# Kernel optimization log

Hardware: AMD Instinct MI355X
Metric: run time of the kernel (lower is better)

The kernel has to match this reference:

```python
import jax, jax.numpy as jnp
import numpy as np

BN_EPS = 1e-5
L2_EPS = 1e-12  # F.normalize eps


def _phi(x, w, gamma, beta, mean, var):
    # 1x1x1 conv (pointwise channel mix) + BatchNorm3d (inference) + ReLU
    # x: (B, C, T, H, W), w: (L, C) -> (B, L, T, H, W)
    y = jnp.einsum('bcthw,lc->blthw', x, w)
    scale = gamma * jax.lax.rsqrt(var + BN_EPS)
    shift = beta - mean * scale
    y = y * scale[None, :, None, None, None] + shift[None, :, None, None, None]
    return jax.nn.relu(y)


def _l2norm(x, axis):
    n = jnp.sqrt(jnp.sum(x * x, axis=axis, keepdims=True))
    return x / jnp.maximum(n, L2_EPS)


def setup_inputs() -> dict:
    key = jax.random.key(0)
    ks = jax.random.split(key, 8)
    B, C, T, H, W = 8, 512, 8, 28, 28
    L = 64
    inp = {
        'query_feature': jax.random.normal(ks[0], (B, C, T, H, W), jnp.float32),
        'key_feature': jax.random.normal(ks[1], (B, C, T, H, W), jnp.float32),
        'phi_w': jax.random.normal(ks[2], (L, C), jnp.float32) * (1.0 / np.sqrt(C)),
        'phi_gamma': jnp.ones((L,), jnp.float32),
        'phi_beta': jnp.zeros((L,), jnp.float32),
        'phi_mean': jax.random.normal(ks[3], (L,), jnp.float32) * 0.1,
        'phi_var': jax.random.uniform(ks[4], (L,), jnp.float32, 0.5, 1.5),
        'phip_w': jax.random.normal(ks[5], (L, C), jnp.float32) * (1.0 / np.sqrt(C)),
        'phip_gamma': jnp.ones((L,), jnp.float32),
        'phip_beta': jnp.zeros((L,), jnp.float32),
        'phip_mean': jax.random.normal(ks[6], (L,), jnp.float32) * 0.1,
        'phip_var': jax.random.uniform(ks[7], (L,), jnp.float32, 0.5, 1.5),
    }
    return inp


def reference(query_feature, key_feature, phi_w, phi_gamma, phi_beta, phi_mean, phi_var,
              phip_w, phip_gamma, phip_beta, phip_mean, phip_var):
    B, C, T, Hk, Wk = key_feature.shape
    _, _, _, Hq, Wq = query_feature.shape
    Nk = T * Hk * Wk
    Nq = T * Hq * Wq

    # visible -> latent adjacency, L2-normalized over spatial-temporal nodes
    a_v2l = _phi(key_feature, phi_w, phi_gamma, phi_beta, phi_mean, phi_var)
    a_v2l = _l2norm(a_v2l.reshape(B, -1, Nk), axis=2)              # (B, L, Nk)

    k = key_feature.reshape(B, C, Nk)
    latent = jnp.einsum('bln,bcn->blc', a_v2l, k)                   # (B, L, C)

    ln = _l2norm(latent, axis=-1)
    aff = jax.nn.softmax(jnp.einsum('blc,bmc->blm', ln, ln), axis=-1)  # (B, L, L)
    latent = jnp.einsum('blm,bmc->blc', aff, latent)                # (B, L, C)

    # latent -> visible adjacency, L2-normalized over latent dim
    a_l2v = _phi(query_feature, phip_w, phip_gamma, phip_beta, phip_mean, phip_var)
    a_l2v = _l2norm(a_l2v.reshape(B, -1, Nq), axis=1)               # (B, L, Nq)

    out = jnp.einsum('blc,bln->bcn', latent, a_l2v)                 # (B, C, Nq)
    return out.reshape(B, C, T, Hq, Wq)
```

## Files before the change

### kernel.cpp

```cpp
#include <hip/hip_runtime.h>
#include <stdint.h>
#include <stddef.h>

#define NB 8
#define NC 512
#define NL 64
#define NN 6272
#define NT 64
#define NTILES (NN / NT)
#define NTA 32
#define NTILES32 (NN / NTA)
#define NCHUNK 14
#define NSUB (NTILES32 / NCHUNK)

typedef short bf16x8 __attribute__((ext_vector_type(8)));
typedef float f32x4 __attribute__((ext_vector_type(4)));

__device__ __forceinline__ unsigned short f2bf(float f) {
    uint32_t u = __float_as_uint(f);
    u += 0x7fffu + ((u >> 16) & 1u);
    return (unsigned short)(u >> 16);
}
__device__ __forceinline__ float bf2f(unsigned short s) {
    return __uint_as_float(((uint32_t)s) << 16);
}

__global__ __launch_bounds__(512)
void kW(const float* __restrict__ w0, const float* __restrict__ w1,
        unsigned short* __restrict__ f0, unsigned short* __restrict__ f1) {
    const float* src = blockIdx.x ? w1 : w0;
    unsigned short* dst = blockIdx.x ? f1 : f0;
    int t = threadIdx.x;
    #pragma unroll
    for (int j = 0; j < 8; j++) {
        int chunk = t + j * 512;
        int r = chunk & 15, q = (chunk >> 4) & 3, it = (chunk >> 6) & 15, lg = chunk >> 10;
        const float* sp = src + (size_t)(lg * 16 + r) * NC + it * 32 + q * 8;
        float4 x = *(const float4*)sp;
        float4 y = *(const float4*)(sp + 4);
        bf16x8 o;
        o[0] = (short)f2bf(x.x); o[1] = (short)f2bf(x.y);
        o[2] = (short)f2bf(x.z); o[3] = (short)f2bf(x.w);
        o[4] = (short)f2bf(y.x); o[5] = (short)f2bf(y.y);
        o[6] = (short)f2bf(y.z); o[7] = (short)f2bf(y.w);
        *(bf16x8*)(dst + (size_t)chunk * 8) = o;
    }
}

__global__ __launch_bounds__(512, 2)
void kAP(const float* __restrict__ key, const unsigned short* __restrict__ wfA,
         const float* __restrict__ gmaA, const float* __restrict__ btaA,
         const float* __restrict__ muA, const float* __restrict__ varA,
         float* __restrict__ part, float* __restrict__ ssqp,
         const float* __restrict__ query, const unsigned short* __restrict__ wfP,
         const float* __restrict__ gmaP, const float* __restrict__ btaP,
         const float* __restrict__ muP, const float* __restrict__ varP,
         unsigned short* __restrict__ a2T) {
    extern __shared__ char smem[];
    const int id = blockIdx.x;
    const int nA = NCHUNK * NB;
    const int tid = threadIdx.x;
    const int w = tid >> 6;
    const int lane = tid & 63;
    const int q = lane >> 4;
    const int r = lane & 15;
    const f32x4 fz = {0.f, 0.f, 0.f, 0.f};

    if (id < nA) {
        unsigned short* Knc = (unsigned short*)smem;
        unsigned short* Kcn = (unsigned short*)(smem + 33280);
        unsigned short* A1  = (unsigned short*)(smem + 74240);
        float* sc = (float*)(smem + 79360);
        float* sh = sc + NL;

        const int chunk = id % NCHUNK;
        const int b     = id / NCHUNK;
        const int n0    = chunk * (NSUB * NTA);

        if (tid < NL) {
            float s = gmaA[tid] * rsqrtf(varA[tid] + 1e-5f);
            sc[tid] = s;
            sh[tid] = btaA[tid] - muA[tid] * s;
        }

        const int l0  = (w & 3) * 16;
        const int nc0 = (w >> 2) * 16;
        const int c0  = w * 64;
        const int na = nc0 + r;
        const int ga = (na >> 2) & 7;
        const unsigned short* wfp = wfA + ((size_t)((w & 3) * 1024 + q * 16 + r)) * 8;

        const int i4  = tid & 7;
        const int cb0 = tid >> 3;
        const float* kpb = key + (size_t)b * NC * NN + n0;

        uint2 pr[8];
        #pragma unroll
        for (int p = 0; p < 8; p++) {
            float4 v = *(const float4*)(kpb + (size_t)(cb0 + 64 * p) * NN + i4 * 4);
            pr[p].x = (uint32_t)f2bf(v.x) | ((uint32_t)f2bf(v.y) << 16);
            pr[p].y = (uint32_t)f2bf(v.z) | ((uint32_t)f2bf(v.w) << 16);
        }

        f32x4 acc2[4][4];
        #pragma unroll
        for (int fm = 0; fm < 4; fm++)
            #pragma unroll
            for (int fc = 0; fc < 4; fc++) acc2[fm][fc] = fz;
        float s_acc = 0.f;

        for (int s = 0; s < NSUB; s++) {
            __syncthreads();

            #pragma unroll
            for (int p = 0; p < 8; p++) {
                int c = cb0 + 64 * p;
                *(uint2*)&Kcn[c * 40 + i4 * 4] = pr[p];
                int cs = (((c >> 3) ^ i4) << 3) | (c & 7);
                int j = i4 * 4;
                Knc[(j + 0) * 520 + cs] = (unsigned short)(pr[p].x);
                Knc[(j + 1) * 520 + cs] = (unsigned short)(pr[p].x >> 16);
                Knc[(j + 2) * 520 + cs] = (unsigned short)(pr[p].y);
                Knc[(j + 3) * 520 + cs] = (unsigned short)(pr[p].y >> 16);
            }
            __syncthreads();

            if (s + 1 < NSUB) {
                const float* kp = kpb + (s + 1) * NTA;
                #pragma unroll
                for (int p = 0; p < 8; p++) {
                    float4 v = *(const float4*)(kp + (size_t)(cb0 + 64 * p) * NN + i4 * 4);
                    pr[p].x = (uint32_t)f2bf(v.x) | ((uint32_t)f2bf(v.y) << 16);
                    pr[p].y = (uint32_t)f2bf(v.z) | ((uint32_t)f2bf(v.w) << 16);
                }
            }

            {
                f32x4 acc0 = fz;
                #pragma unroll
                for (int it = 0; it < 16; it++) {
                    bf16x8 af = *(const bf16x8*)&wfp[it * 512];
                    bf16x8 b0 = *(const bf16x8*)&Knc[na * 520 + (((it * 4 + q) ^ ga) << 3)];
                    acc0 = __builtin_amdgcn_mfma_f32_16x16x32_bf16(b0, af, acc0, 0, 0, 0);
                }
                const int l = l0 + r;
                const float scl = sc[l], shf = sh[l];
                ushort4 t;
                float v0 = fmaxf(acc0[0] * scl + shf, 0.f);
                float v1 = fmaxf(acc0[1] * scl + shf, 0.f);
                float v2 = fmaxf(acc0[2] * scl + shf, 0.f);
                float v3 = fmaxf(acc0[3] * scl + shf, 0.f);
                t.x = f2bf(v0); t.y = f2bf(v1); t.z = f2bf(v2); t.w = f2bf(v3);
                s_acc += v0 * v0 + v1 * v1 + v2 * v2 + v3 * v3;
                *(ushort4*)&A1[l * 40 + nc0 + q * 4] = t;
            }
            __syncthreads();

            {
                bf16x8 a[4];
                #pragma unroll
                for (int fm = 0; fm < 4; fm++)
                    a[fm] = *(const bf16x8*)&A1[(fm * 16 + r) * 40 + q * 8];
                #pragma unroll
                for (int fc = 0; fc < 4; fc++) {
                    bf16x8 bb = *(const bf16x8*)&Kcn[(c0 + fc * 16 + r) * 40 + q * 8];
                    #pragma unroll
                    for (int fm = 0; fm < 4; fm++)
                        acc2[fm][fc] = __builtin_amdgcn_mfma_f32_16x16x32_bf16(bb, a[fm], acc2[fm][fc], 0, 0, 0);
                }
            }
        }

        {
            float s = s_acc;
            s += __shfl_xor(s, 16);
            s += __shfl_xor(s, 32);
            float* sp = ssqp + (((size_t)(chunk * NB + b) * 2 + (w >> 2))) * NL;
            if (lane < 16) sp[l0 + lane] = s;
        }

        float* wp2 = part + ((size_t)(chunk * NB + b) * 8 + w) * 4096 + lane * 4;
        #pragma unroll
        for (int fm = 0; fm < 4; fm++)
            #pragma unroll
            for (int fc = 0; fc < 4; fc++)
                *(f32x4*)(wp2 + (fm * 4 + fc) * 256) = acc2[fm][fc];
    } else {
        unsigned short* Qnc = (unsigned short*)smem;
        unsigned short* A2  = (unsigned short*)(smem + 33280);
        float* ssn = (float*)(smem + 33280 + 4608);
        float* sc = ssn + 32;
        float* sh = sc + 64;

        const int pid = id - nA;
        const int b   = pid / NTILES32;
        const int n0  = (pid % NTILES32) * NTA;

        if (tid < 64) {
            float s = gmaP[tid] * rsqrtf(varP[tid] + 1e-5f);
            sc[tid] = s;
            sh[tid] = btaP[tid] - muP[tid] * s;
        }
        if (tid < 32) ssn[tid] = 0.f;

        const int i4  = tid & 7;
        const int cb0 = tid >> 3;
        const float* qp = query + (size_t)b * NC * NN + n0;
        #pragma unroll
        for (int p = 0; p < 8; p++) {
            int c = cb0 + 64 * p;
            float4 v = *(const float4*)(qp + (size_t)c * NN + i4 * 4);
            int cs = (((c >> 3) ^ i4) << 3) | (c & 7);
            int j = i4 * 4;
            Qnc[(j + 0) * 520 + cs] = f2bf(v.x);
            Qnc[(j + 1) * 520 + cs] = f2bf(v.y);
            Qnc[(j + 2) * 520 + cs] = f2bf(v.z);
            Qnc[(j + 3) * 520 + cs] = f2bf(v.w);
        }
        __syncthreads();

        const int l0 = (w & 3) * 16, nc0 = (w >> 2) * 16;
        const int na = nc0 + r;
        const int ga = (na >> 2) & 7;
        const unsigned short* wfp = wfP + ((size_t)((w & 3) * 1024 + q * 16 + r)) * 8;

        f32x4 acc0 = fz;
        #pragma unroll
        for (int it = 0; it < 16; it++) {
            bf16x8 af = *(const bf16x8*)&wfp[it * 512];
            bf16x8 b0 = *(const bf16x8*)&Qnc[na * 520 + (((it * 4 + q) ^ ga) << 3)];
            acc0 = __builtin_amdgcn_mfma_f32_16x16x32_bf16(af, b0, acc0, 0, 0, 0);
        }

        float s0 = 0.f;
        {
            unsigned short t0[4];
            #pragma unroll
            for (int i = 0; i < 4; i++) {
                int l = l0 + q * 4 + i;
                float v0 = fmaxf(acc0[i] * sc[l] + sh[l], 0.f);
                t0[i] = f2bf(v0);
                s0 += v0 * v0;
            }
            *(ushort4*)&A2[na * 72 + l0 + 4 * q] = make_ushort4(t0[0], t0[1], t0[2], t0[3]);
        }

        s0 += __shfl_xor(s0, 16);
        s0 += __shfl_xor(s0, 32);
        if (lane < 16) atomicAdd(&ssn[na], s0);
        __syncthreads();

        if (tid < 256) {
            int row = tid >> 3, ch = tid & 7;
            float inv = 1.f / fmaxf(sqrtf(ssn[row]), 1e-12f);
            bf16x8 x = *(const bf16x8*)&A2[row * 72 + ch * 8];
            bf16x8 o;
            #pragma unroll
            for (int k = 0; k < 8; k++)
                o[k] = (short)f2bf(bf2f((unsigned short)x[k]) * inv);
            *(bf16x8*)&a2T[((size_t)b * NN + n0 + row) * 64 + ch * 8] = o;
        }
    }
}

__global__ __launch_bounds__(256)
void kR(const float* __restrict__ part, float* __restrict__ latu) {
    int gid = blockIdx.x * 256 + threadIdx.x;
    int lane = gid & 63;
    int fc = (gid >> 6) & 3;
    int fm = (gid >> 8) & 3;
    int w  = (gid >> 10) & 7;
    int b  = gid >> 13;
    int q = lane >> 4, r = lane & 15;

    const float* src = part + ((size_t)(b * 8 + w) * 16 + fm * 4 + fc) * 256 + lane * 4;
    f32x4 acc = {0.f, 0.f, 0.f, 0.f};
    for (int ch = 0; ch < NCHUNK; ch++) {
        f32x4 v = *(const f32x4*)(src + (size_t)ch * (NB * 8 * 4096));
        acc += v;
    }
    float* dst = latu + ((size_t)(b * 64 + fm * 16 + r)) * NC + w * 64 + fc * 16 + q * 4;
    *(f32x4*)dst = acc;
}

__global__ __launch_bounds__(256, 1)
void kB(const float* __restrict__ latu, const float* __restrict__ ssqp,
        unsigned short* __restrict__ lat2T) {
    extern __shared__ char smem[];
    unsigned short* Lb = (unsigned short*)smem;
    unsigned short* Lt = (unsigned short*)(smem + 66560);
    float* aff = (float*)(smem + 140288);
    float* inv_nl = (float*)(smem + 157696);
    float* s_c = inv_nl + 64;

    const int tid = threadIdx.x;
    const int b = blockIdx.x;

    if (tid < 64) {
        float s = 0.f;
        for (int ch = 0; ch < NCHUNK; ch++) {
            size_t base = (((size_t)ch * NB + b) * 2) * NL + tid;
            s += ssqp[base] + ssqp[base + NL];
        }
        inv_nl[tid] = 1.f / fmaxf(sqrtf(s), 1e-12f);
    }
    __syncthreads();

    const float* lu = latu + (size_t)b * NL * NC;
    for (int idx = tid; idx < NL * (NC / 4); idx += 256) {
        int l = idx >> 7;
        int c = (idx & 127) << 2;
        float4 v = *(const float4*)(lu + l * NC + c);
        float inv = inv_nl[l];
        unsigned short b0 = f2bf(v.x * inv), b1 = f2bf(v.y * inv);
        unsigned short b2 = f2bf(v.z * inv), b3 = f2bf(v.w * inv);
        uint32_t* d = (uint32_t*)&Lb[l * 520 + c];
        d[0] = (uint32_t)b0 | ((uint32_t)b1 << 16);
        d[1] = (uint32_t)b2 | ((uint32_t)b3 << 16);
        Lt[(c + 0) * 72 + l] = b0;
        Lt[(c + 1) * 72 + l] = b1;
        Lt[(c + 2) * 72 + l] = b2;
        Lt[(c + 3) * 72 + l] = b3;
    }
    __syncthreads();

    {
        int l = tid >> 2, p = tid & 3;
        float s = 0.f;
        for (int c = p * 128; c < p * 128 + 128; c += 4) {
            const unsigned short* d = &Lb[l * 520 + c];
            float v0 = bf2f(d[0]), v1 = bf2f(d[1]), v2 = bf2f(d[2]), v3 = bf2f(d[3]);
            s += v0 * v0 + v1 * v1 + v2 * v2 + v3 * v3;
        }
        s += __shfl_xor(s, 1);
        s += __shfl_xor(s, 2);
        if (p == 0) s_c[l] = 1.f / fmaxf(sqrtf(s), 1e-12f);
    }
    __syncthreads();

    const int w = tid >> 6, lane = tid & 63, q = lane >> 4, r = lane & 15;
    const f32x4 fz = {0.f, 0.f, 0.f, 0.f};

    {
        f32x4 g[4];
        #pragma unroll
        for (int fm = 0; fm < 4; fm++) g[fm] = fz;
        for (int kc = 0; kc < NC; kc += 32) {
            bf16x8 a = *(const bf16x8*)&Lb[(w * 16 + r) * 520 + kc + q * 8];
            #pragma unroll
            for (int fm = 0; fm < 4; fm++) {
                bf16x8 bb = *(const bf16x8*)&Lb[(fm * 16 + r) * 520 + kc + q * 8];
                g[fm] = __builtin_amdgcn_mfma_f32_16x16x32_bf16(a, bb, g[fm], 0, 0, 0);
            }
        }
        #pragma unroll
        for (int fm = 0; fm < 4; fm++)
            #pragma unroll
            for (int i = 0; i < 4; i++) {
                int l = w * 16 + q * 4 + i;
                int m = fm * 16 + r;
                aff[l * 68 + m] = g[fm][i] * s_c[l] * s_c[m];
            }
    }
    __syncthreads();

    {
        int l = tid >> 2, p = tid & 3;
        float e[16];
        float mx = -1e30f;
        #pragma unroll
        for (int k = 0; k < 16; k++) mx = fmaxf(mx, aff[l * 68 + p * 16 + k]);
        mx = fmaxf(mx, __shfl_xor(mx, 1));
        mx = fmaxf(mx, __shfl_xor(mx, 2));
        float s = 0.f;
        #pragma unroll
        for (int k = 0; k < 16; k++) { e[k] = __expf(aff[l * 68 + p * 16 + k] - mx); s += e[k]; }
        s += __shfl_xor(s, 1);
        s += __shfl_xor(s, 2);
        float invs = 1.f / s;
        __syncthreads();
        #pragma unroll
        for (int k = 0; k < 16; k++) aff[l * 68 + p * 16 + k] = e[k] * invs;
    }
    __syncthreads();

    {
        f32x4 acc[4][8];
        #pragma unroll
        for (int fm = 0; fm < 4; fm++)
            #pragma unroll
            for (int fc = 0; fc < 8; fc++) acc[fm][fc] = fz;
        #pragma unroll
        for (int km = 0; km < 64; km += 32) {
            bf16x8 a[4];
            #pragma unroll
            for (int fm = 0; fm < 4; fm++) {
                const float* ap = &aff[(fm * 16 + r) * 68 + km + q * 8];
                float4 x = *(const float4*)ap;
                float4 y = *(const float4*)(ap + 4);
                bf16x8 t;
                t[0] = (short)f2bf(x.x); t[1] = (short)f2bf(x.y);
                t[2] = (short)f2bf(x.z); t[3] = (short)f2bf(x.w);
                t[4] = (short)f2bf(y.x); t[5] = (short)f2bf(y.y);
                t[6] = (short)f2bf(y.z); t[7] = (short)f2bf(y.w);
                a[fm] = t;
            }
            #pragma unroll
            for (int fc = 0; fc < 8; fc++) {
                bf16x8 bb = *(const bf16x8*)&Lt[(w * 128 + fc * 16 + r) * 72 + km + q * 8];
                #pragma unroll
                for (int fm = 0; fm < 4; fm++)
                    acc[fm][fc] = __builtin_amdgcn_mfma_f32_16x16x32_bf16(a[fm], bb, acc[fm][fc], 0, 0, 0);
            }
        }
        unsigned short* out = lat2T + (size_t)b * NC * NL;
        #pragma unroll
        for (int fm = 0; fm < 4; fm++)
            #pragma unroll
            for (int fc = 0; fc < 8; fc++)
                #pragma unroll
                for (int i = 0; i < 4; i++) {
                    int l = fm * 16 + q * 4 + i;
                    int c = w * 128 + fc * 16 + r;
                    out[c * 64 + l] = f2bf(acc[fm][fc][i]);
                }
    }
}

__global__ __launch_bounds__(256, 4)
void kC3(const unsigned short* __restrict__ a2T,
         const unsigned short* __restrict__ lat2T, float* __restrict__ out) {
    __shared__ unsigned short At[64 * 72];
    __shared__ float Bnc[4][16][68];

    const int tid = threadIdx.x;
    const int b = blockIdx.y;
    const int n0 = blockIdx.x * NT;

    const unsigned short* src = a2T + ((size_t)b * NN + n0) * 64;
    #pragma unroll
    for (int k = 0; k < 2; k++) {
        int idx = tid + k * 256;
        int row = idx >> 3, ch = idx & 7;
        *(uint4*)&At[row * 72 + ch * 8] = *(const uint4*)&src[row * 64 + ch * 8];
    }
    __syncthreads();

    const int w = tid >> 6, lane = tid & 63, q = lane >> 4, r = lane & 15;
    const f32x4 fz = {0.f, 0.f, 0.f, 0.f};
    const unsigned short* Ab = lat2T + (size_t)b * NC * NL;
    float* op = out + (size_t)b * NC * NN + n0;

    #pragma unroll
    for (int half = 0; half < 2; half++) {
        int cb = w * 128 + half * 64;
        f32x4 acc[4][4];
        #pragma unroll
        for (int fm = 0; fm < 4; fm++)
            #pragma unroll
            for (int fn = 0; fn < 4; fn++) acc[fm][fn] = fz;
        #pragma unroll
        for (int kl = 0; kl < 64; kl += 32) {
            bf16x8 a[4];
            #pragma unroll
            for (int fm = 0; fm < 4; fm++)
                a[fm] = *(const bf16x8*)&Ab[(size_t)(cb + fm * 16 + r) * 64 + kl + q * 8];
            #pragma unroll
            for (int fn = 0; fn < 4; fn++) {
                bf16x8 bb = *(const bf16x8*)&At[(fn * 16 + r) * 72 + kl + q * 8];
                #pragma unroll
                for (int fm = 0; fm < 4; fm++)
                    acc[fm][fn] = __builtin_amdgcn_mfma_f32_16x16x32_bf16(bb, a[fm], acc[fm][fn], 0, 0, 0);
            }
        }
        #pragma unroll
        for (int fm = 0; fm < 4; fm++) {
            #pragma unroll
            for (int fn = 0; fn < 4; fn++)
                *(f32x4*)&Bnc[w][r][fn * 16 + q * 4] = acc[fm][fn];
            #pragma unroll
            for (int rb = 0; rb < 4; rb++) {
                int crow = rb * 4 + (lane >> 4);
                f32x4 v = *(const f32x4*)&Bnc[w][crow][(lane & 15) * 4];
                *(f32x4*)(op + (size_t)(cb + fm * 16 + crow) * NN + (lane & 15) * 4) = v;
            }
        }
    }
}

extern "C" void kernel_launch(void* const* d_in, const int* in_sizes, int n_in,
                              void* d_out, int out_size, void* d_ws, size_t ws_size,
                              hipStream_t stream) {
    (void)in_sizes; (void)n_in; (void)out_size; (void)ws_size;
    const float* query = (const float*)d_in[0];
    const float* key   = (const float*)d_in[1];
    const float* phi_w = (const float*)d_in[2];
    const float* phi_g = (const float*)d_in[3];
    const float* phi_b = (const float*)d_in[4];
    const float* phi_m = (const float*)d_in[5];
    const float* phi_v = (const float*)d_in[6];
    const float* php_w = (const float*)d_in[7];
    const float* php_g = (const float*)d_in[8];
    const float* php_b = (const float*)d_in[9];
    const float* php_m = (const float*)d_in[10];
    const float* php_v = (const float*)d_in[11];
    float* out = (float*)d_out;

    char* ws = (char*)d_ws;
    size_t off = 0;
    float* part = (float*)(ws + off);           off += (size_t)NCHUNK * NB * NL * NC * 4;
    float* ssqp = (float*)(ws + off);           off += (size_t)NCHUNK * NB * 2 * NL * 4;
    float* latu = (float*)(ws + off);           off += 1048576;
    unsigned short* lat2T = (unsigned short*)(ws + off); off += 524288;
    unsigned short* a2T   = (unsigned short*)(ws + off); off += 6422528;
    unsigned short* wfA   = (unsigned short*)(ws + off); off += 65536;
    unsigned short* wfP   = (unsigned short*)(ws + off); off += 65536;

    (void)hipFuncSetAttribute((const void*)kAP, hipFuncAttributeMaxDynamicSharedMemorySize, 79872);
    (void)hipFuncSetAttribute((const void*)kB, hipFuncAttributeMaxDynamicSharedMemorySize, 158208);

    kW<<<dim3(2), 512, 0, stream>>>(phi_w, php_w, wfA, wfP);
    int nblocks = NCHUNK * NB + NTILES32 * NB;
    kAP<<<dim3(nblocks), 512, 79872, stream>>>(key, wfA, phi_g, phi_b, phi_m, phi_v,
                                               part, ssqp,
                                               query, wfP, php_g, php_b, php_m, php_v, a2T);
    kR<<<dim3(256), 256, 0, stream>>>(part, latu);
    kB<<<dim3(NB), 256, 158208, stream>>>(latu, ssqp, lat2T);
    kC3<<<dim3(NTILES, NB), 256, 0, stream>>>(a2T, lat2T, out);
}
```

Before: 135.1 us.

## Double kAP tile width to 64 nodes with 1024-thread blocks

```diff
diff --git a/kernel.cpp b/kernel.cpp
--- a/kernel.cpp
+++ b/kernel.cpp
@@ -8,10 +8,8 @@
 #define NN 6272
 #define NT 64
 #define NTILES (NN / NT)
-#define NTA 32
-#define NTILES32 (NN / NTA)
 #define NCHUNK 14
-#define NSUB (NTILES32 / NCHUNK)
+#define NSUB (NTILES / NCHUNK)
 
 typedef short bf16x8 __attribute__((ext_vector_type(8)));
 typedef float f32x4 __attribute__((ext_vector_type(4)));
@@ -47,7 +45,7 @@
     }
 }
 
-__global__ __launch_bounds__(512, 2)
+__global__ __launch_bounds__(1024, 1)
 void kAP(const float* __restrict__ key, const unsigned short* __restrict__ wfA,
          const float* __restrict__ gmaA, const float* __restrict__ btaA,
          const float* __restrict__ muA, const float* __restrict__ varA,
@@ -65,17 +63,25 @@
     const int q = lane >> 4;
     const int r = lane & 15;
     const f32x4 fz = {0.f, 0.f, 0.f, 0.f};
+    const int lg = w & 3;
+    const int ng = w >> 2;
+    const int l0 = lg * 16;
+    const int ngc0 = ng * 16;
+    const int na = ngc0 + r;
+    const int ga = (na >> 2) & 7;
+    const int i4  = tid & 15;
+    const int cb0 = tid >> 4;
 
     if (id < nA) {
         unsigned short* Knc = (unsigned short*)smem;
-        unsigned short* Kcn = (unsigned short*)(smem + 33280);
-        unsigned short* A1  = (unsigned short*)(smem + 74240);
-        float* sc = (float*)(smem + 79360);
+        unsigned short* Kcn = (unsigned short*)(smem + 66560);
+        unsigned short* A1  = (unsigned short*)(smem + 140288);
+        float* sc = (float*)(smem + 149504);
         float* sh = sc + NL;
 
         const int chunk = id % NCHUNK;
         const int b     = id / NCHUNK;
-        const int n0    = chunk * (NSUB * NTA);
+        const int n0    = chunk * (NSUB * NT);
 
         if (tid < NL) {
             float s = gmaA[tid] * rsqrtf(varA[tid] + 1e-5f);
@@ -83,15 +89,7 @@
             sh[tid] = btaA[tid] - muA[tid] * s;
         }
 
-        const int l0  = (w & 3) * 16;
-        const int nc0 = (w >> 2) * 16;
-        const int c0  = w * 64;
-        const int na = nc0 + r;
-        const int ga = (na >> 2) & 7;
-        const unsigned short* wfp = wfA + ((size_t)((w & 3) * 1024 + q * 16 + r)) * 8;
-
-        const int i4  = tid & 7;
-        const int cb0 = tid >> 3;
+        const unsigned short* wfp = wfA + ((size_t)(lg * 1024 + q * 16 + r)) * 8;
         const float* kpb = key + (size_t)b * NC * NN + n0;
 
         uint2 pr[8];
@@ -102,11 +100,11 @@
             pr[p].y = (uint32_t)f2bf(v.z) | ((uint32_t)f2bf(v.w) << 16);
         }
 
-        f32x4 acc2[4][4];
+        f32x4 acc2[4][2];
         #pragma unroll
         for (int fm = 0; fm < 4; fm++)
             #pragma unroll
-            for (int fc = 0; fc < 4; fc++) acc2[fm][fc] = fz;
+            for (int fc = 0; fc < 2; fc++) acc2[fm][fc] = fz;
         float s_acc = 0.f;
 
         for (int s = 0; s < NSUB; s++) {
@@ -115,8 +113,8 @@
             #pragma unroll
             for (int p = 0; p < 8; p++) {
                 int c = cb0 + 64 * p;
-                *(uint2*)&Kcn[c * 40 + i4 * 4] = pr[p];
-                int cs = (((c >> 3) ^ i4) << 3) | (c & 7);
+                *(uint2*)&Kcn[c * 72 + i4 * 4] = pr[p];
+                int cs = (((c >> 3) ^ (i4 & 7)) << 3) | (c & 7);
                 int j = i4 * 4;
                 Knc[(j + 0) * 520 + cs] = (unsigned short)(pr[p].x);
                 Knc[(j + 1) * 520 + cs] = (unsigned short)(pr[p].x >> 16);
@@ -126,7 +124,7 @@
             __syncthreads();
 
             if (s + 1 < NSUB) {
-                const float* kp = kpb + (s + 1) * NTA;
+                const float* kp = kpb + (s + 1) * NT;
                 #pragma unroll
                 for (int p = 0; p < 8; p++) {
                     float4 v = *(const float4*)(kp + (size_t)(cb0 + 64 * p) * NN + i4 * 4);
@@ -152,21 +150,25 @@
                 float v3 = fmaxf(acc0[3] * scl + shf, 0.f);
                 t.x = f2bf(v0); t.y = f2bf(v1); t.z = f2bf(v2); t.w = f2bf(v3);
                 s_acc += v0 * v0 + v1 * v1 + v2 * v2 + v3 * v3;
-                *(ushort4*)&A1[l * 40 + nc0 + q * 4] = t;
+                *(ushort4*)&A1[l * 72 + ngc0 + q * 4] = t;
             }
             __syncthreads();
 
             {
-                bf16x8 a[4];
+                const int c0 = w * 32;
                 #pragma unroll
-                for (int fm = 0; fm < 4; fm++)
-                    a[fm] = *(const bf16x8*)&A1[(fm * 16 + r) * 40 + q * 8];
-                #pragma unroll
-                for (int fc = 0; fc < 4; fc++) {
-                    bf16x8 bb = *(const bf16x8*)&Kcn[(c0 + fc * 16 + r) * 40 + q * 8];
+                for (int kn = 0; kn < NT; kn += 32) {
+                    bf16x8 a[4];
                     #pragma unroll
                     for (int fm = 0; fm < 4; fm++)
-                        acc2[fm][fc] = __builtin_amdgcn_mfma_f32_16x16x32_bf16(bb, a[fm], acc2[fm][fc], 0, 0, 0);
+                        a[fm] = *(const bf16x8*)&A1[(fm * 16 + r) * 72 + kn + q * 8];
+                    #pragma unroll
+                    for (int fc = 0; fc < 2; fc++) {
+                        bf16x8 bb = *(const bf16x8*)&Kcn[(c0 + fc * 16 + r) * 72 + kn + q * 8];
+                        #pragma unroll
+                        for (int fm = 0; fm < 4; fm++)
+                            acc2[fm][fc] = __builtin_amdgcn_mfma_f32_16x16x32_bf16(bb, a[fm], acc2[fm][fc], 0, 0, 0);
+                    }
                 }
             }
         }
@@ -175,42 +177,40 @@
             float s = s_acc;
             s += __shfl_xor(s, 16);
             s += __shfl_xor(s, 32);
-            float* sp = ssqp + (((size_t)(chunk * NB + b) * 2 + (w >> 2))) * NL;
+            float* sp = ssqp + (((size_t)(chunk * NB + b) * 4 + ng)) * NL;
             if (lane < 16) sp[l0 + lane] = s;
         }
 
-        float* wp2 = part + ((size_t)(chunk * NB + b) * 8 + w) * 4096 + lane * 4;
+        float* wp2 = part + ((size_t)(chunk * NB + b)) * 32768 + w * 2048 + lane * 4;
         #pragma unroll
         for (int fm = 0; fm < 4; fm++)
             #pragma unroll
-            for (int fc = 0; fc < 4; fc++)
-                *(f32x4*)(wp2 + (fm * 4 + fc) * 256) = acc2[fm][fc];
+            for (int fc = 0; fc < 2; fc++)
+                *(f32x4*)(wp2 + (fm * 2 + fc) * 256) = acc2[fm][fc];
     } else {
         unsigned short* Qnc = (unsigned short*)smem;
-        unsigned short* A2  = (unsigned short*)(smem + 33280);
-        float* ssn = (float*)(smem + 33280 + 4608);
-        float* sc = ssn + 32;
+        unsigned short* A2  = (unsigned short*)(smem + 66560);
+        float* ssn = (float*)(smem + 66560 + 9216);
+        float* sc = ssn + 64;
         float* sh = sc + 64;
 
         const int pid = id - nA;
-        const int b   = pid / NTILES32;
-        const int n0  = (pid % NTILES32) * NTA;
+        const int b   = pid / NTILES;
+        const int n0  = (pid % NTILES) * NT;
 
         if (tid < 64) {
             float s = gmaP[tid] * rsqrtf(varP[tid] + 1e-5f);
             sc[tid] = s;
             sh[tid] = btaP[tid] - muP[tid] * s;
-        }
-        if (tid < 32) ssn[tid] = 0.f;
-
-        const int i4  = tid & 7;
-        const int cb0 = tid >> 3;
+            ssn[tid] = 0.f;
+        }
+
         const float* qp = query + (size_t)b * NC * NN + n0;
         #pragma unroll
         for (int p = 0; p < 8; p++) {
             int c = cb0 + 64 * p;
             float4 v = *(const float4*)(qp + (size_t)c * NN + i4 * 4);
-            int cs = (((c >> 3) ^ i4) << 3) | (c & 7);
+            int cs = (((c >> 3) ^ (i4 & 7)) << 3) | (c & 7);
             int j = i4 * 4;
             Qnc[(j + 0) * 520 + cs] = f2bf(v.x);
             Qnc[(j + 1) * 520 + cs] = f2bf(v.y);
@@ -219,10 +219,7 @@
         }
         __syncthreads();
 
-        const int l0 = (w & 3) * 16, nc0 = (w >> 2) * 16;
-        const int na = nc0 + r;
-        const int ga = (na >> 2) & 7;
-        const unsigned short* wfp = wfP + ((size_t)((w & 3) * 1024 + q * 16 + r)) * 8;
+        const unsigned short* wfp = wfP + ((size_t)(lg * 1024 + q * 16 + r)) * 8;
 
         f32x4 acc0 = fz;
         #pragma unroll
@@ -250,7 +247,7 @@
         if (lane < 16) atomicAdd(&ssn[na], s0);
         __syncthreads();
 
-        if (tid < 256) {
+        if (tid < 512) {
             int row = tid >> 3, ch = tid & 7;
             float inv = 1.f / fmaxf(sqrtf(ssn[row]), 1e-12f);
             bf16x8 x = *(const bf16x8*)&A2[row * 72 + ch * 8];
@@ -267,19 +264,19 @@
 void kR(const float* __restrict__ part, float* __restrict__ latu) {
     int gid = blockIdx.x * 256 + threadIdx.x;
     int lane = gid & 63;
-    int fc = (gid >> 6) & 3;
-    int fm = (gid >> 8) & 3;
-    int w  = (gid >> 10) & 7;
+    int fc = (gid >> 6) & 1;
+    int fm = (gid >> 7) & 3;
+    int w  = (gid >> 9) & 15;
     int b  = gid >> 13;
     int q = lane >> 4, r = lane & 15;
 
-    const float* src = part + ((size_t)(b * 8 + w) * 16 + fm * 4 + fc) * 256 + lane * 4;
+    const float* src = part + (size_t)b * 32768 + w * 2048 + (fm * 2 + fc) * 256 + lane * 4;
     f32x4 acc = {0.f, 0.f, 0.f, 0.f};
     for (int ch = 0; ch < NCHUNK; ch++) {
-        f32x4 v = *(const f32x4*)(src + (size_t)ch * (NB * 8 * 4096));
+        f32x4 v = *(const f32x4*)(src + (size_t)ch * (NB * 32768));
         acc += v;
     }
-    float* dst = latu + ((size_t)(b * 64 + fm * 16 + r)) * NC + w * 64 + fc * 16 + q * 4;
+    float* dst = latu + ((size_t)(b * 64 + fm * 16 + r)) * NC + w * 32 + fc * 16 + q * 4;
     *(f32x4*)dst = acc;
 }
 
@@ -299,8 +296,8 @@
     if (tid < 64) {
         float s = 0.f;
         for (int ch = 0; ch < NCHUNK; ch++) {
-            size_t base = (((size_t)ch * NB + b) * 2) * NL + tid;
-            s += ssqp[base] + ssqp[base + NL];
+            size_t base = (((size_t)ch * NB + b) * 4) * NL + tid;
+            s += ssqp[base] + ssqp[base + NL] + ssqp[base + 2 * NL] + ssqp[base + 3 * NL];
         }
         inv_nl[tid] = 1.f / fmaxf(sqrtf(s), 1e-12f);
     }
@@ -509,21 +506,21 @@
     char* ws = (char*)d_ws;
     size_t off = 0;
     float* part = (float*)(ws + off);           off += (size_t)NCHUNK * NB * NL * NC * 4;
-    float* ssqp = (float*)(ws + off);           off += (size_t)NCHUNK * NB * 2 * NL * 4;
+    float* ssqp = (float*)(ws + off);           off += (size_t)NCHUNK * NB * 4 * NL * 4;
     float* latu = (float*)(ws + off);           off += 1048576;
     unsigned short* lat2T = (unsigned short*)(ws + off); off += 524288;
     unsigned short* a2T   = (unsigned short*)(ws + off); off += 6422528;
     unsigned short* wfA   = (unsigned short*)(ws + off); off += 65536;
     unsigned short* wfP   = (unsigned short*)(ws + off); off += 65536;
 
-    (void)hipFuncSetAttribute((const void*)kAP, hipFuncAttributeMaxDynamicSharedMemorySize, 79872);
+    (void)hipFuncSetAttribute((const void*)kAP, hipFuncAttributeMaxDynamicSharedMemorySize, 150016);
     (void)hipFuncSetAttribute((const void*)kB, hipFuncAttributeMaxDynamicSharedMemorySize, 158208);
 
     kW<<<dim3(2), 512, 0, stream>>>(phi_w, php_w, wfA, wfP);
-    int nblocks = NCHUNK * NB + NTILES32 * NB;
-    kAP<<<dim3(nblocks), 512, 79872, stream>>>(key, wfA, phi_g, phi_b, phi_m, phi_v,
-                                               part, ssqp,
-                                               query, wfP, php_g, php_b, php_m, php_v, a2T);
+    int nblocks = NCHUNK * NB + NTILES * NB;
+    kAP<<<dim3(nblocks), 1024, 150016, stream>>>(key, wfA, phi_g, phi_b, phi_m, phi_v,
+                                                 part, ssqp,
+                                                 query, wfP, php_g, php_b, php_m, php_v, a2T);
     kR<<<dim3(256), 256, 0, stream>>>(part, latu);
     kB<<<dim3(NB), 256, 158208, stream>>>(latu, ssqp, lat2T);
     kC3<<<dim3(NTILES, NB), 256, 0, stream>>>(a2T, lat2T, out);
```

New measurement: 178.9 us. 1.32x slower.

## Defer bf16 conversion of prefetched key tiles and batch query loads

Applied to the files above, without the earlier changes.

```diff
diff --git a/kernel.cpp b/kernel.cpp
--- a/kernel.cpp
+++ b/kernel.cpp
@@ -47,7 +47,7 @@
     }
 }
 
-__global__ __launch_bounds__(512, 2)
+__global__ __launch_bounds__(512, 1)
 void kAP(const float* __restrict__ key, const unsigned short* __restrict__ wfA,
          const float* __restrict__ gmaA, const float* __restrict__ btaA,
          const float* __restrict__ muA, const float* __restrict__ varA,
@@ -94,13 +94,10 @@
         const int cb0 = tid >> 3;
         const float* kpb = key + (size_t)b * NC * NN + n0;
 
-        uint2 pr[8];
-        #pragma unroll
-        for (int p = 0; p < 8; p++) {
-            float4 v = *(const float4*)(kpb + (size_t)(cb0 + 64 * p) * NN + i4 * 4);
-            pr[p].x = (uint32_t)f2bf(v.x) | ((uint32_t)f2bf(v.y) << 16);
-            pr[p].y = (uint32_t)f2bf(v.z) | ((uint32_t)f2bf(v.w) << 16);
-        }
+        float4 prv[8];
+        #pragma unroll
+        for (int p = 0; p < 8; p++)
+            prv[p] = *(const float4*)(kpb + (size_t)(cb0 + 64 * p) * NN + i4 * 4);
 
         f32x4 acc2[4][4];
         #pragma unroll
@@ -115,24 +112,24 @@
             #pragma unroll
             for (int p = 0; p < 8; p++) {
                 int c = cb0 + 64 * p;
-                *(uint2*)&Kcn[c * 40 + i4 * 4] = pr[p];
+                uint2 pk;
+                pk.x = (uint32_t)f2bf(prv[p].x) | ((uint32_t)f2bf(prv[p].y) << 16);
+                pk.y = (uint32_t)f2bf(prv[p].z) | ((uint32_t)f2bf(prv[p].w) << 16);
+                *(uint2*)&Kcn[c * 40 + i4 * 4] = pk;
                 int cs = (((c >> 3) ^ i4) << 3) | (c & 7);
                 int j = i4 * 4;
-                Knc[(j + 0) * 520 + cs] = (unsigned short)(pr[p].x);
-                Knc[(j + 1) * 520 + cs] = (unsigned short)(pr[p].x >> 16);
-                Knc[(j + 2) * 520 + cs] = (unsigned short)(pr[p].y);
-                Knc[(j + 3) * 520 + cs] = (unsigned short)(pr[p].y >> 16);
+                Knc[(j + 0) * 520 + cs] = (unsigned short)(pk.x);
+                Knc[(j + 1) * 520 + cs] = (unsigned short)(pk.x >> 16);
+                Knc[(j + 2) * 520 + cs] = (unsigned short)(pk.y);
+                Knc[(j + 3) * 520 + cs] = (unsigned short)(pk.y >> 16);
             }
             __syncthreads();
 
             if (s + 1 < NSUB) {
                 const float* kp = kpb + (s + 1) * NTA;
                 #pragma unroll
-                for (int p = 0; p < 8; p++) {
-                    float4 v = *(const float4*)(kp + (size_t)(cb0 + 64 * p) * NN + i4 * 4);
-                    pr[p].x = (uint32_t)f2bf(v.x) | ((uint32_t)f2bf(v.y) << 16);
-                    pr[p].y = (uint32_t)f2bf(v.z) | ((uint32_t)f2bf(v.w) << 16);
-                }
+                for (int p = 0; p < 8; p++)
+                    prv[p] = *(const float4*)(kp + (size_t)(cb0 + 64 * p) * NN + i4 * 4);
             }
 
             {
@@ -206,16 +203,19 @@
         const int i4  = tid & 7;
         const int cb0 = tid >> 3;
         const float* qp = query + (size_t)b * NC * NN + n0;
+        float4 qv[8];
+        #pragma unroll
+        for (int p = 0; p < 8; p++)
+            qv[p] = *(const float4*)(qp + (size_t)(cb0 + 64 * p) * NN + i4 * 4);
         #pragma unroll
         for (int p = 0; p < 8; p++) {
             int c = cb0 + 64 * p;
-            float4 v = *(const float4*)(qp + (size_t)c * NN + i4 * 4);
             int cs = (((c >> 3) ^ i4) << 3) | (c & 7);
             int j = i4 * 4;
-            Qnc[(j + 0) * 520 + cs] = f2bf(v.x);
-            Qnc[(j + 1) * 520 + cs] = f2bf(v.y);
-            Qnc[(j + 2) * 520 + cs] = f2bf(v.z);
-            Qnc[(j + 3) * 520 + cs] = f2bf(v.w);
+            Qnc[(j + 0) * 520 + cs] = f2bf(qv[p].x);
+            Qnc[(j + 1) * 520 + cs] = f2bf(qv[p].y);
+            Qnc[(j + 2) * 520 + cs] = f2bf(qv[p].z);
+            Qnc[(j + 3) * 520 + cs] = f2bf(qv[p].w);
         }
         __syncthreads();
 
```

Result: faster. 115.9 us (-14.2%).
